# Kernel optimization log

Hardware: AMD Instinct MI355X
Metric: run time of the kernel (lower is better)

Reference implementation:

```python
import jax, jax.numpy as jnp
import numpy as np

N_NODES = 50000
N_EDGES = 640000
IN_FEATS = 128
HID = 128


def setup_inputs() -> dict:
    key = jax.random.key(0)
    ks = jax.random.split(key, 8)
    x = jax.random.normal(ks[0], (N_NODES, IN_FEATS), dtype=jnp.float32)
    src = jax.random.randint(ks[1], (N_EDGES,), 0, N_NODES, dtype=jnp.int32)
    dst = jax.random.randint(ks[2], (N_EDGES,), 0, N_NODES, dtype=jnp.int32)
    s1 = 1.0 / np.sqrt(IN_FEATS)
    s2 = 1.0 / np.sqrt(HID)
    W1 = jax.random.normal(ks[3], (IN_FEATS, HID), dtype=jnp.float32) * s1
    b1 = jnp.zeros((HID,), dtype=jnp.float32)
    W2 = jax.random.normal(ks[4], (HID, HID), dtype=jnp.float32) * s2
    b2 = jnp.zeros((HID,), dtype=jnp.float32)
    Wr = jax.random.normal(ks[5], (HID, 2), dtype=jnp.float32) * s2
    br = jnp.zeros((2,), dtype=jnp.float32)
    return {"x": x, "src": src, "dst": dst, "W1": W1, "b1": b1,
            "W2": W2, "b2": b2, "Wr": Wr, "br": br}


def _degree_norm(idx, n):
    # D^{-1/2}, with 0 for zero-degree nodes (DGL sets inf -> 0)
    deg = jax.ops.segment_sum(jnp.ones(idx.shape[0], jnp.float32), idx, num_segments=n)
    return jnp.where(deg > 0, jax.lax.rsqrt(jnp.maximum(deg, 1.0)), 0.0)


def _graph_conv(h, W, b, src, dst, norm_out, norm_in, n):
    # DGL GraphConv, norm='both': out = D_in^{-1/2} A D_out^{-1/2} (h W) + b
    hW = (h * norm_out[:, None]) @ W          # [N, hid]
    agg = jax.ops.segment_sum(hW[src], dst, num_segments=n)  # gather+scatter over edges
    return agg * norm_in[:, None] + b


def reference(x, src, dst, W1, b1, W2, b2, Wr, br):
    n = x.shape[0]
    norm_out = _degree_norm(src, n)  # source-side out-degree norm
    norm_in = _degree_norm(dst, n)   # dest-side in-degree norm
    h = jax.nn.relu(_graph_conv(x, W1, b1, src, dst, norm_out, norm_in, n))
    h = jax.nn.relu(_graph_conv(h, W2, b2, src, dst, norm_out, norm_in, n))
    hg = jnp.mean(h, axis=0, keepdims=True)  # [1, hid]
    return hg @ Wr + br                      # [1, 2]
```

## Files before the change

### kernel.cpp

```cpp
#include <hip/hip_runtime.h>
#include <hip/hip_bf16.h>

#define FEAT 128
#define RBITS 12
#define RSIZE 4096
#define NCHUNK 64

typedef __attribute__((ext_vector_type(8))) short short8;
typedef __attribute__((ext_vector_type(4))) short short4v;
typedef __attribute__((ext_vector_type(4))) float f32x4;

__device__ __forceinline__ ushort f2bf(float f) {
    union { float f; unsigned u; } v; v.f = f;
    unsigned u = v.u;
    unsigned r = 0x7fffu + ((u >> 16) & 1u);
    return (ushort)((u + r) >> 16);
}
__device__ __forceinline__ float bf2f(short s) {
    union { unsigned u; float f; } v;
    v.u = ((unsigned)(ushort)s) << 16;
    return v.f;
}

__global__ __launch_bounds__(256)
void hist_kernel(const int* __restrict__ src, const int* __restrict__ dst,
                 unsigned* __restrict__ partial, int E, int CS)
{
    __shared__ unsigned hist[RSIZE];
    const int c = blockIdx.x, p = blockIdx.y, job = blockIdx.z;
    const int* __restrict__ idx = job ? dst : src;
    for (int r = threadIdx.x; r < RSIZE; r += 256) hist[r] = 0;
    __syncthreads();
    const int e0 = c * CS, e1 = min(E, e0 + CS);
    for (int e = e0 + threadIdx.x; e < e1; e += 256) {
        int v = idx[e];
        if ((v >> RBITS) == p) atomicAdd(&hist[v & (RSIZE - 1)], 1u);
    }
    __syncthreads();
    unsigned* out = partial +
        (((size_t)job * gridDim.y + p) * NCHUNK + c) * RSIZE;
    for (int r = threadIdx.x; r < RSIZE; r += 256) out[r] = hist[r];
}

__global__ __launch_bounds__(256)
void merge_kernel(unsigned* __restrict__ partialOut, unsigned* __restrict__ partialIn,
                  int* __restrict__ cntIn, float* __restrict__ normOut,
                  float* __restrict__ normIn, int N)
{
    int n = blockIdx.x * 256 + threadIdx.x;
    if (n >= N) return;
    const int p = n >> RBITS, r = n & (RSIZE - 1);
    const size_t base = (size_t)p * NCHUNK * RSIZE + r;
    unsigned so = 0;
#pragma unroll 8
    for (int c = 0; c < NCHUNK; ++c) so += partialOut[base + (size_t)c * RSIZE];
    unsigned off = 0;
#pragma unroll 8
    for (int c = 0; c < NCHUNK; ++c) {
        size_t i = base + (size_t)c * RSIZE;
        unsigned t = partialIn[i];
        partialIn[i] = off;
        off += t;
    }
    cntIn[n]   = (int)off;
    normIn[n]  = off ? rsqrtf((float)off) : 0.0f;
    normOut[n] = so  ? rsqrtf((float)so)  : 0.0f;
}

__global__ __launch_bounds__(256)
void scan1_kernel(const int* __restrict__ cnt, int* __restrict__ blockSums, int N)
{
    __shared__ int sh[256];
    int i = blockIdx.x * 256 + threadIdx.x;
    sh[threadIdx.x] = (i < N) ? cnt[i] : 0;
    __syncthreads();
    for (int off = 128; off > 0; off >>= 1) {
        if (threadIdx.x < off) sh[threadIdx.x] += sh[threadIdx.x + off];
        __syncthreads();
    }
    if (threadIdx.x == 0) blockSums[blockIdx.x] = sh[0];
}

__global__ __launch_bounds__(256)
void rowstart_kernel(const int* __restrict__ cntIn, const int* __restrict__ blockSums,
                     int* __restrict__ rowStart, int N, int NB, int E)
{
    __shared__ int bs[256];
    __shared__ int bse[256];
    __shared__ int sh[256];
    const int t = threadIdx.x;
    int bv = (t < NB) ? blockSums[t] : 0;
    bs[t] = bv;
    __syncthreads();
    for (int off = 1; off < 256; off <<= 1) {
        int u = (t >= off) ? bs[t - off] : 0;
        __syncthreads();
        bs[t] += u;
        __syncthreads();
    }
    bse[t] = bs[t] - bv;
    __syncthreads();

    const int i = blockIdx.x * 256 + t;
    int v = (i < N) ? cntIn[i] : 0;
    sh[t] = v;
    __syncthreads();
    for (int off = 1; off < 256; off <<= 1) {
        int u = (t >= off) ? sh[t - off] : 0;
        __syncthreads();
        sh[t] += u;
        __syncthreads();
    }
    if (i < N) rowStart[i] = bse[blockIdx.x] + sh[t] - v;
    if (blockIdx.x == 0 && t == 0) rowStart[N] = E;
}

__global__ __launch_bounds__(256)
void fill_kernel(const int* __restrict__ src, const int* __restrict__ dst,
                 const int* __restrict__ rowStart, const unsigned* __restrict__ chunkOff,
                 int* __restrict__ csrSrc, int N, int E, int CS)
{
    __shared__ unsigned cursor[RSIZE];
    const int c = blockIdx.x, p = blockIdx.y;
    const unsigned* co = chunkOff + ((size_t)p * NCHUNK + c) * RSIZE;
    for (int r = threadIdx.x; r < RSIZE; r += 256) {
        int n = (p << RBITS) + r;
        cursor[r] = (n < N) ? (unsigned)rowStart[n] + co[r] : 0u;
    }
    __syncthreads();
    const int e0 = c * CS, e1 = min(E, e0 + CS);
    for (int e = e0 + threadIdx.x; e < e1; e += 256) {
        int d = dst[e];
        if ((d >> RBITS) == p) {
            unsigned pos = atomicAdd(&cursor[d & (RSIZE - 1)], 1u);
            csrSrc[pos] = src[e];
        }
    }
}

template<bool F32IN>
__global__ __launch_bounds__(256)
void gemm_mfma_kernel(const void* __restrict__ Ain, const float* __restrict__ W,
                      const float* __restrict__ scale, ushort* __restrict__ C,
                      int M, int nStrips)
{
    __shared__ ushort WT[128 * 132];
    __shared__ ushort As[64 * 132];
    __shared__ float  sScale[64];

    const int tid  = threadIdx.x;
    const int wv   = tid >> 6;
    const int lane = tid & 63;
    const int rowHalf = wv >> 1;
    const int colHalf = wv & 1;
    const int l15  = lane & 15;
    const int quad = lane >> 4;

    for (int it = 0; it < 16; ++it) {
        int fid = tid + (it << 8);
        int k   = fid >> 5;
        int c4  = (fid & 31) << 2;
        float4 w = *(const float4*)(W + (size_t)k * FEAT + c4);
        WT[(c4 + 0) * 132 + k] = f2bf(w.x);
        WT[(c4 + 1) * 132 + k] = f2bf(w.y);
        WT[(c4 + 2) * 132 + k] = f2bf(w.z);
        WT[(c4 + 3) * 132 + k] = f2bf(w.w);
    }
    __syncthreads();

    short8 bfrag[4][4];
#pragma unroll
    for (int ct = 0; ct < 4; ++ct) {
        int col = colHalf * 64 + ct * 16 + l15;
#pragma unroll
        for (int kst = 0; kst < 4; ++kst) {
            int k = kst * 32 + quad * 8;
            short4v lo = *(const short4v*)&WT[col * 132 + k];
            short4v hi = *(const short4v*)&WT[col * 132 + k + 4];
            bfrag[ct][kst] = __builtin_shufflevector(lo, hi, 0, 1, 2, 3, 4, 5, 6, 7);
        }
    }

    for (int s = blockIdx.x; s < nStrips; s += gridDim.x) {
        const int row0 = s << 6;
        __syncthreads();

#pragma unroll
        for (int it = 0; it < 4; ++it) {
            int fid = tid + (it << 8);
            int r   = fid >> 4;
            int seg = (fid & 15) << 3;
            int grow = row0 + r;
            short4v lo = {0, 0, 0, 0}, hi = {0, 0, 0, 0};
            if (grow < M) {
                if (F32IN) {
                    const float* pa = (const float*)Ain + (size_t)grow * FEAT + seg;
                    float4 u0 = *(const float4*)(pa);
                    float4 u1 = *(const float4*)(pa + 4);
                    lo[0] = (short)f2bf(u0.x); lo[1] = (short)f2bf(u0.y);
                    lo[2] = (short)f2bf(u0.z); lo[3] = (short)f2bf(u0.w);
                    hi[0] = (short)f2bf(u1.x); hi[1] = (short)f2bf(u1.y);
                    hi[2] = (short)f2bf(u1.z); hi[3] = (short)f2bf(u1.w);
                } else {
                    const ushort* pa = (const ushort*)Ain + (size_t)grow * FEAT + seg;
                    lo = *(const short4v*)(pa);
                    hi = *(const short4v*)(pa + 4);
                }
            }
            *(short4v*)&As[r * 132 + seg]     = lo;
            *(short4v*)&As[r * 132 + seg + 4] = hi;
        }
        if (tid < 64) {
            int grow = row0 + tid;
            sScale[tid] = (grow < M) ? scale[grow] : 0.0f;
        }
        __syncthreads();

        f32x4 acc[2][4] = {};
#pragma unroll
        for (int kst = 0; kst < 4; ++kst) {
            int k = kst * 32 + quad * 8;
            short8 af[2];
#pragma unroll
            for (int rt = 0; rt < 2; ++rt) {
                int row = rowHalf * 32 + rt * 16 + l15;
                short4v lo = *(const short4v*)&As[row * 132 + k];
                short4v hi = *(const short4v*)&As[row * 132 + k + 4];
                af[rt] = __builtin_shufflevector(lo, hi, 0, 1, 2, 3, 4, 5, 6, 7);
            }
#pragma unroll
            for (int rt = 0; rt < 2; ++rt)
#pragma unroll
                for (int ct = 0; ct < 4; ++ct)
                    acc[rt][ct] = __builtin_amdgcn_mfma_f32_16x16x32_bf16(
                        af[rt], bfrag[ct][kst], acc[rt][ct], 0, 0, 0);
        }

#pragma unroll
        for (int rt = 0; rt < 2; ++rt) {
            int rbase = rowHalf * 32 + rt * 16 + quad * 4;
#pragma unroll
            for (int reg = 0; reg < 4; ++reg) {
                int rl = rbase + reg;
                int grow = row0 + rl;
                if (grow < M) {
                    float sc = sScale[rl];
#pragma unroll
                    for (int ct = 0; ct < 4; ++ct) {
                        int col = colHalf * 64 + ct * 16 + l15;
                        C[(size_t)grow * FEAT + col] = f2bf(acc[rt][ct][reg] * sc);
                    }
                }
            }
        }
    }
}

__global__ __launch_bounds__(256)
void gather_kernel(const ushort* __restrict__ t, const int* __restrict__ rowStart,
                   const int* __restrict__ csrSrc, const float* __restrict__ normIn,
                   const float* __restrict__ bias, ushort* __restrict__ out, int N)
{
    const int hw   = threadIdx.x >> 5;
    const int lane = threadIdx.x & 31;
    const int node = blockIdx.x * 8 + hw;
    if (node >= N) return;
    const int s = rowStart[node];
    const int e = rowStart[node + 1];
    float a0 = 0.f, a1 = 0.f, a2 = 0.f, a3 = 0.f;
    for (int base = s; base < e; base += 32) {
        const int m = min(32, e - base);
        int idx = (base + lane < e) ? csrSrc[base + lane] : 0;
        int j = 0;
        for (; j + 4 <= m; j += 4) {
            int s0 = __shfl(idx, j,     32);
            int s1 = __shfl(idx, j + 1, 32);
            int s2 = __shfl(idx, j + 2, 32);
            int s3 = __shfl(idx, j + 3, 32);
            short4v v0 = *(const short4v*)(t + (size_t)s0 * FEAT + lane * 4);
            short4v v1 = *(const short4v*)(t + (size_t)s1 * FEAT + lane * 4);
            short4v v2 = *(const short4v*)(t + (size_t)s2 * FEAT + lane * 4);
            short4v v3 = *(const short4v*)(t + (size_t)s3 * FEAT + lane * 4);
            a0 += bf2f(v0[0]) + bf2f(v1[0]) + bf2f(v2[0]) + bf2f(v3[0]);
            a1 += bf2f(v0[1]) + bf2f(v1[1]) + bf2f(v2[1]) + bf2f(v3[1]);
            a2 += bf2f(v0[2]) + bf2f(v1[2]) + bf2f(v2[2]) + bf2f(v3[2]);
            a3 += bf2f(v0[3]) + bf2f(v1[3]) + bf2f(v2[3]) + bf2f(v3[3]);
        }
        for (; j < m; ++j) {
            int srcn = __shfl(idx, j, 32);
            short4v v = *(const short4v*)(t + (size_t)srcn * FEAT + lane * 4);
            a0 += bf2f(v[0]); a1 += bf2f(v[1]); a2 += bf2f(v[2]); a3 += bf2f(v[3]);
        }
    }
    float ni = normIn[node];
    float4 b = *(const float4*)(bias + lane * 4);
    short4v o;
    o[0] = (short)f2bf(fmaxf(fmaf(a0, ni, b.x), 0.0f));
    o[1] = (short)f2bf(fmaxf(fmaf(a1, ni, b.y), 0.0f));
    o[2] = (short)f2bf(fmaxf(fmaf(a2, ni, b.z), 0.0f));
    o[3] = (short)f2bf(fmaxf(fmaf(a3, ni, b.w), 0.0f));
    *(short4v*)(out + (size_t)node * FEAT + lane * 4) = o;
}

__global__ __launch_bounds__(256)
void colreduce_kernel(const ushort* __restrict__ h2, float* __restrict__ colsum, int N)
{
    const int c  = threadIdx.x & 127;
    const int rg = threadIdx.x >> 7;
    const int r0 = blockIdx.x * 256;
    const int rEnd = min(r0 + 256, N);
    float acc = 0.0f;
    for (int r = r0 + rg; r < rEnd; r += 2)
        acc += bf2f(h2[(size_t)r * FEAT + c]);
    __shared__ float sh[256];
    sh[threadIdx.x] = acc;
    __syncthreads();
    if (rg == 0) unsafeAtomicAdd(&colsum[c], sh[c] + sh[128 + c]);
}

__global__ __launch_bounds__(128)
void final_kernel(const float* __restrict__ colsum, const float* __restrict__ Wr,
                  const float* __restrict__ br, float* __restrict__ out, float invN)
{
    __shared__ float s0[128], s1[128];
    int j = threadIdx.x;
    float hg = colsum[j] * invN;
    s0[j] = hg * Wr[2 * j + 0];
    s1[j] = hg * Wr[2 * j + 1];
    __syncthreads();
    for (int off = 64; off > 0; off >>= 1) {
        if (j < off) { s0[j] += s0[j + off]; s1[j] += s1[j + off]; }
        __syncthreads();
    }
    if (j == 0) {
        out[0] = s0[0] + br[0];
        out[1] = s1[0] + br[1];
    }
}

extern "C" void kernel_launch(void* const* d_in, const int* in_sizes, int n_in,
                              void* d_out, int out_size, void* d_ws, size_t ws_size,
                              hipStream_t stream)
{
    const float* x   = (const float*)d_in[0];
    const int*   src = (const int*)d_in[1];
    const int*   dst = (const int*)d_in[2];
    const float* W1  = (const float*)d_in[3];
    const float* b1  = (const float*)d_in[4];
    const float* W2  = (const float*)d_in[5];
    const float* b2  = (const float*)d_in[6];
    const float* Wr  = (const float*)d_in[7];
    const float* br  = (const float*)d_in[8];
    float* out = (float*)d_out;

    const int N = in_sizes[0] / FEAT;
    const int E = in_sizes[1];
    const int NP = ((N + 255) / 256) * 256;
    const int NB = (N + 255) / 256;
    const int P  = (N + RSIZE - 1) / RSIZE;
    const int CS = (E + NCHUNK - 1) / NCHUNK;

    char* p = (char*)d_ws;
    unsigned* partial   = (unsigned*)p;  p += (size_t)2 * P * NCHUNK * RSIZE * 4;
    float*  colsum    = (float*)p;       p += 256 * 4;
    int*    blockSums = (int*)p;         p += 256 * 4;
    int*    cntIn     = (int*)p;         p += (size_t)NP * 4;
    float*  normOut   = (float*)p;       p += (size_t)NP * 4;
    float*  normIn    = (float*)p;       p += (size_t)NP * 4;
    int*    rowStart  = (int*)p;         p += (size_t)(NP + 64) * 4;
    int*    csrSrc    = (int*)p;         p += (size_t)E * 4;
    ushort* bufT      = (ushort*)p;      p += (size_t)N * FEAT * 2;
    ushort* bufH      = (ushort*)p;      p += (size_t)N * FEAT * 2;

    unsigned* partialOut = partial;
    unsigned* partialIn  = partial + (size_t)P * NCHUNK * RSIZE;

    hipMemsetAsync(colsum, 0, 256 * 4, stream);

    hist_kernel<<<dim3(NCHUNK, P, 2), 256, 0, stream>>>(src, dst, partial, E, CS);
    merge_kernel<<<NB, 256, 0, stream>>>(partialOut, partialIn, cntIn, normOut, normIn, N);
    scan1_kernel<<<NB, 256, 0, stream>>>(cntIn, blockSums, N);
    rowstart_kernel<<<NB, 256, 0, stream>>>(cntIn, blockSums, rowStart, N, NB, E);
    fill_kernel<<<dim3(NCHUNK, P), 256, 0, stream>>>(src, dst, rowStart, partialIn, csrSrc, N, E, CS);

    const int nStrips = (N + 63) / 64;
    const int gathBlocks = (N + 7) / 8;

    gemm_mfma_kernel<true><<<256, 256, 0, stream>>>((const void*)x, W1, normOut, bufT, N, nStrips);
    gather_kernel<<<gathBlocks, 256, 0, stream>>>(bufT, rowStart, csrSrc, normIn, b1, bufH, N);

    gemm_mfma_kernel<false><<<256, 256, 0, stream>>>((const void*)bufH, W2, normOut, bufT, N, nStrips);
    gather_kernel<<<gathBlocks, 256, 0, stream>>>(bufT, rowStart, csrSrc, normIn, b2, bufH, N);

    colreduce_kernel<<<NB, 256, 0, stream>>>(bufH, colsum, N);
    final_kernel<<<1, 128, 0, stream>>>(colsum, Wr, br, out, 1.0f / (float)N);
}
```

Baseline: 258.3 us.

## Vectorize hist/fill loads, fuse scan into merge, widen gather loads, retune radix

The histogram and fill kernels now read edge indices four at a time with int4 loads, and the bin radix is doubled while the chunk count is halved, so fewer partial histograms are written and merged. The block-sum scan is folded into the merge kernel, which removes one launch. The gather kernel now has each half-warp load 16-byte rows for two neighbours at once and combines the halves with a shuffle, so each load is wider and more loads are in flight. The larger LDS histogram (32 KB) may lower occupancy, and the chunk size is rounded up to a multiple of four to keep the int4 loads aligned.

```diff
diff --git a/kernel.cpp b/kernel.cpp
--- a/kernel.cpp
+++ b/kernel.cpp
@@ -2,9 +2,9 @@
 #include <hip/hip_bf16.h>
 
 #define FEAT 128
-#define RBITS 12
-#define RSIZE 4096
-#define NCHUNK 64
+#define RBITS 13
+#define RSIZE 8192
+#define NCHUNK 32
 
 typedef __attribute__((ext_vector_type(8))) short short8;
 typedef __attribute__((ext_vector_type(4))) short short4v;
@@ -32,50 +32,53 @@
     for (int r = threadIdx.x; r < RSIZE; r += 256) hist[r] = 0;
     __syncthreads();
     const int e0 = c * CS, e1 = min(E, e0 + CS);
-    for (int e = e0 + threadIdx.x; e < e1; e += 256) {
+    const int eA = e0 + ((e1 - e0) & ~3);
+    for (int e = e0 + threadIdx.x * 4; e + 4 <= e1; e += 1024) {
+        int4 v = *(const int4*)(idx + e);
+        if ((v.x >> RBITS) == p) atomicAdd(&hist[v.x & (RSIZE - 1)], 1u);
+        if ((v.y >> RBITS) == p) atomicAdd(&hist[v.y & (RSIZE - 1)], 1u);
+        if ((v.z >> RBITS) == p) atomicAdd(&hist[v.z & (RSIZE - 1)], 1u);
+        if ((v.w >> RBITS) == p) atomicAdd(&hist[v.w & (RSIZE - 1)], 1u);
+    }
+    for (int e = eA + threadIdx.x; e < e1; e += 256) {
         int v = idx[e];
         if ((v >> RBITS) == p) atomicAdd(&hist[v & (RSIZE - 1)], 1u);
     }
     __syncthreads();
-    unsigned* out = partial +
+    unsigned* outp = partial +
         (((size_t)job * gridDim.y + p) * NCHUNK + c) * RSIZE;
-    for (int r = threadIdx.x; r < RSIZE; r += 256) out[r] = hist[r];
-}
-
-__global__ __launch_bounds__(256)
-void merge_kernel(unsigned* __restrict__ partialOut, unsigned* __restrict__ partialIn,
+    for (int r = threadIdx.x; r < RSIZE; r += 256) outp[r] = hist[r];
+}
+
+__global__ __launch_bounds__(256)
+void merge_kernel(const unsigned* __restrict__ partialOut, unsigned* __restrict__ partialIn,
                   int* __restrict__ cntIn, float* __restrict__ normOut,
-                  float* __restrict__ normIn, int N)
-{
-    int n = blockIdx.x * 256 + threadIdx.x;
-    if (n >= N) return;
-    const int p = n >> RBITS, r = n & (RSIZE - 1);
-    const size_t base = (size_t)p * NCHUNK * RSIZE + r;
-    unsigned so = 0;
+                  float* __restrict__ normIn, int* __restrict__ blockSums, int N)
+{
+    __shared__ int sh[256];
+    const int n = blockIdx.x * 256 + threadIdx.x;
+    unsigned off = 0;
+    if (n < N) {
+        const int p = n >> RBITS, r = n & (RSIZE - 1);
+        const size_t base = (size_t)p * NCHUNK * RSIZE + r;
+        unsigned so = 0;
 #pragma unroll 8
-    for (int c = 0; c < NCHUNK; ++c) so += partialOut[base + (size_t)c * RSIZE];
-    unsigned off = 0;
+        for (int c = 0; c < NCHUNK; ++c) so += partialOut[base + (size_t)c * RSIZE];
 #pragma unroll 8
-    for (int c = 0; c < NCHUNK; ++c) {
-        size_t i = base + (size_t)c * RSIZE;
-        unsigned t = partialIn[i];
-        partialIn[i] = off;
-        off += t;
-    }
-    cntIn[n]   = (int)off;
-    normIn[n]  = off ? rsqrtf((float)off) : 0.0f;
-    normOut[n] = so  ? rsqrtf((float)so)  : 0.0f;
-}
-
-__global__ __launch_bounds__(256)
-void scan1_kernel(const int* __restrict__ cnt, int* __restrict__ blockSums, int N)
-{
-    __shared__ int sh[256];
-    int i = blockIdx.x * 256 + threadIdx.x;
-    sh[threadIdx.x] = (i < N) ? cnt[i] : 0;
-    __syncthreads();
-    for (int off = 128; off > 0; off >>= 1) {
-        if (threadIdx.x < off) sh[threadIdx.x] += sh[threadIdx.x + off];
+        for (int c = 0; c < NCHUNK; ++c) {
+            size_t i = base + (size_t)c * RSIZE;
+            unsigned t = partialIn[i];
+            partialIn[i] = off;
+            off += t;
+        }
+        cntIn[n]   = (int)off;
+        normIn[n]  = off ? rsqrtf((float)off) : 0.0f;
+        normOut[n] = so  ? rsqrtf((float)so)  : 0.0f;
+    }
+    sh[threadIdx.x] = (int)off;
+    __syncthreads();
+    for (int o = 128; o > 0; o >>= 1) {
+        if (threadIdx.x < o) sh[threadIdx.x] += sh[threadIdx.x + o];
         __syncthreads();
     }
     if (threadIdx.x == 0) blockSums[blockIdx.x] = sh[0];
@@ -129,12 +132,17 @@
     }
     __syncthreads();
     const int e0 = c * CS, e1 = min(E, e0 + CS);
-    for (int e = e0 + threadIdx.x; e < e1; e += 256) {
+    const int eA = e0 + ((e1 - e0) & ~3);
+    for (int e = e0 + threadIdx.x * 4; e + 4 <= e1; e += 1024) {
+        int4 d = *(const int4*)(dst + e);
+        if ((d.x >> RBITS) == p) { unsigned q = atomicAdd(&cursor[d.x & (RSIZE - 1)], 1u); csrSrc[q] = src[e]; }
+        if ((d.y >> RBITS) == p) { unsigned q = atomicAdd(&cursor[d.y & (RSIZE - 1)], 1u); csrSrc[q] = src[e + 1]; }
+        if ((d.z >> RBITS) == p) { unsigned q = atomicAdd(&cursor[d.z & (RSIZE - 1)], 1u); csrSrc[q] = src[e + 2]; }
+        if ((d.w >> RBITS) == p) { unsigned q = atomicAdd(&cursor[d.w & (RSIZE - 1)], 1u); csrSrc[q] = src[e + 3]; }
+    }
+    for (int e = eA + threadIdx.x; e < e1; e += 256) {
         int d = dst[e];
-        if ((d >> RBITS) == p) {
-            unsigned pos = atomicAdd(&cursor[d & (RSIZE - 1)], 1u);
-            csrSrc[pos] = src[e];
-        }
+        if ((d >> RBITS) == p) { unsigned q = atomicAdd(&cursor[d & (RSIZE - 1)], 1u); csrSrc[q] = src[e]; }
     }
 }
 
@@ -261,45 +269,53 @@
                    const int* __restrict__ csrSrc, const float* __restrict__ normIn,
                    const float* __restrict__ bias, ushort* __restrict__ out, int N)
 {
-    const int hw   = threadIdx.x >> 5;
+    const int g    = threadIdx.x >> 5;
     const int lane = threadIdx.x & 31;
-    const int node = blockIdx.x * 8 + hw;
+    const int h    = lane >> 4;
+    const int li   = lane & 15;
+    const int node = blockIdx.x * 8 + g;
     if (node >= N) return;
     const int s = rowStart[node];
     const int e = rowStart[node + 1];
-    float a0 = 0.f, a1 = 0.f, a2 = 0.f, a3 = 0.f;
+    float a[8] = {0.f, 0.f, 0.f, 0.f, 0.f, 0.f, 0.f, 0.f};
     for (int base = s; base < e; base += 32) {
         const int m = min(32, e - base);
         int idx = (base + lane < e) ? csrSrc[base + lane] : 0;
-        int j = 0;
-        for (; j + 4 <= m; j += 4) {
-            int s0 = __shfl(idx, j,     32);
-            int s1 = __shfl(idx, j + 1, 32);
-            int s2 = __shfl(idx, j + 2, 32);
-            int s3 = __shfl(idx, j + 3, 32);
-            short4v v0 = *(const short4v*)(t + (size_t)s0 * FEAT + lane * 4);
-            short4v v1 = *(const short4v*)(t + (size_t)s1 * FEAT + lane * 4);
-            short4v v2 = *(const short4v*)(t + (size_t)s2 * FEAT + lane * 4);
-            short4v v3 = *(const short4v*)(t + (size_t)s3 * FEAT + lane * 4);
-            a0 += bf2f(v0[0]) + bf2f(v1[0]) + bf2f(v2[0]) + bf2f(v3[0]);
-            a1 += bf2f(v0[1]) + bf2f(v1[1]) + bf2f(v2[1]) + bf2f(v3[1]);
-            a2 += bf2f(v0[2]) + bf2f(v1[2]) + bf2f(v2[2]) + bf2f(v3[2]);
-            a3 += bf2f(v0[3]) + bf2f(v1[3]) + bf2f(v2[3]) + bf2f(v3[3]);
-        }
-        for (; j < m; ++j) {
-            int srcn = __shfl(idx, j, 32);
-            short4v v = *(const short4v*)(t + (size_t)srcn * FEAT + lane * 4);
-            a0 += bf2f(v[0]); a1 += bf2f(v[1]); a2 += bf2f(v[2]); a3 += bf2f(v[3]);
-        }
-    }
-    float ni = normIn[node];
-    float4 b = *(const float4*)(bias + lane * 4);
-    short4v o;
-    o[0] = (short)f2bf(fmaxf(fmaf(a0, ni, b.x), 0.0f));
-    o[1] = (short)f2bf(fmaxf(fmaf(a1, ni, b.y), 0.0f));
-    o[2] = (short)f2bf(fmaxf(fmaf(a2, ni, b.z), 0.0f));
-    o[3] = (short)f2bf(fmaxf(fmaf(a3, ni, b.w), 0.0f));
-    *(short4v*)(out + (size_t)node * FEAT + lane * 4) = o;
+        for (int j0 = 0; j0 < m; j0 += 8) {
+            const int jh = j0 + h;
+            int s0 = __shfl(idx, jh,     32);
+            int s1 = __shfl(idx, jh + 2, 32);
+            int s2 = __shfl(idx, jh + 4, 32);
+            int s3 = __shfl(idx, jh + 6, 32);
+            short8 v0 = {0,0,0,0,0,0,0,0}, v1 = {0,0,0,0,0,0,0,0};
+            short8 v2 = {0,0,0,0,0,0,0,0}, v3 = {0,0,0,0,0,0,0,0};
+            if (jh     < m) v0 = *(const short8*)(t + (size_t)s0 * FEAT + li * 8);
+            if (jh + 2 < m) v1 = *(const short8*)(t + (size_t)s1 * FEAT + li * 8);
+            if (jh + 4 < m) v2 = *(const short8*)(t + (size_t)s2 * FEAT + li * 8);
+            if (jh + 6 < m) v3 = *(const short8*)(t + (size_t)s3 * FEAT + li * 8);
+#pragma unroll
+            for (int k = 0; k < 8; ++k)
+                a[k] += (bf2f(v0[k]) + bf2f(v1[k])) + (bf2f(v2[k]) + bf2f(v3[k]));
+        }
+    }
+#pragma unroll
+    for (int k = 0; k < 8; ++k)
+        a[k] += __shfl_xor(a[k], 16, 32);
+    if (h == 0) {
+        float ni = normIn[node];
+        float4 b0 = *(const float4*)(bias + li * 8);
+        float4 b1 = *(const float4*)(bias + li * 8 + 4);
+        short8 o;
+        o[0] = (short)f2bf(fmaxf(fmaf(a[0], ni, b0.x), 0.0f));
+        o[1] = (short)f2bf(fmaxf(fmaf(a[1], ni, b0.y), 0.0f));
+        o[2] = (short)f2bf(fmaxf(fmaf(a[2], ni, b0.z), 0.0f));
+        o[3] = (short)f2bf(fmaxf(fmaf(a[3], ni, b0.w), 0.0f));
+        o[4] = (short)f2bf(fmaxf(fmaf(a[4], ni, b1.x), 0.0f));
+        o[5] = (short)f2bf(fmaxf(fmaf(a[5], ni, b1.y), 0.0f));
+        o[6] = (short)f2bf(fmaxf(fmaf(a[6], ni, b1.z), 0.0f));
+        o[7] = (short)f2bf(fmaxf(fmaf(a[7], ni, b1.w), 0.0f));
+        *(short8*)(out + (size_t)node * FEAT + li * 8) = o;
+    }
 }
 
 __global__ __launch_bounds__(256)
@@ -358,10 +374,10 @@
     const int NP = ((N + 255) / 256) * 256;
     const int NB = (N + 255) / 256;
     const int P  = (N + RSIZE - 1) / RSIZE;
-    const int CS = (E + NCHUNK - 1) / NCHUNK;
+    const int CS = (((E + NCHUNK - 1) / NCHUNK) + 3) & ~3;
 
     char* p = (char*)d_ws;
-    unsigned* partial   = (unsigned*)p;  p += (size_t)2 * P * NCHUNK * RSIZE * 4;
+    unsigned* partial = (unsigned*)p;    p += (size_t)2 * P * NCHUNK * RSIZE * 4;
     float*  colsum    = (float*)p;       p += 256 * 4;
     int*    blockSums = (int*)p;         p += 256 * 4;
     int*    cntIn     = (int*)p;         p += (size_t)NP * 4;
@@ -378,8 +394,7 @@
     hipMemsetAsync(colsum, 0, 256 * 4, stream);
 
     hist_kernel<<<dim3(NCHUNK, P, 2), 256, 0, stream>>>(src, dst, partial, E, CS);
-    merge_kernel<<<NB, 256, 0, stream>>>(partialOut, partialIn, cntIn, normOut, normIn, N);
-    scan1_kernel<<<NB, 256, 0, stream>>>(cntIn, blockSums, N);
+    merge_kernel<<<NB, 256, 0, stream>>>(partialOut, partialIn, cntIn, normOut, normIn, blockSums, N);
     rowstart_kernel<<<NB, 256, 0, stream>>>(cntIn, blockSums, rowStart, N, NB, E);
     fill_kernel<<<dim3(NCHUNK, P), 256, 0, stream>>>(src, dst, rowStart, partialIn, csrSrc, N, E, CS);
 
```

Result: faster. 248.3 us (-3.9%).
